# Optimization experiments

Hardware: AMD Instinct MI355X
Metric: run time of the kernel (lower is better)

Reference implementation:

```python
import jax, jax.numpy as jnp
import numpy as np
from jax import lax

WIN = 9  # NCC window per axis (default [9]*3)

# 3x3x3 edge/shape kernels, shape [O=1, I=1, 3, 3, 3]
_LAP = np.zeros((3, 3, 3), np.float32)
_LAP[1, 1, 1] = 6.0
_LAP[0, 1, 1] = _LAP[2, 1, 1] = -1.0
_LAP[1, 0, 1] = _LAP[1, 2, 1] = -1.0
_LAP[1, 1, 0] = _LAP[1, 1, 2] = -1.0
LAP_K = jnp.asarray(_LAP)[None, None]

_row = np.array([[-1.0, 0.0, 1.0], [-2.0, 0.0, 2.0], [-1.0, 0.0, 1.0]], np.float32)
SOBEL_X = jnp.asarray(np.stack([_row, _row, _row], axis=0))[None, None]
_plane = np.array([[-1.0, -2.0, -1.0], [-1.0, -2.0, -1.0], [-1.0, -2.0, -1.0]], np.float32)
SOBEL_Y = jnp.asarray(np.stack([_plane, np.zeros((3, 3), np.float32), -_plane], axis=0))[None, None]
_zp = np.array([[-1.0, -1.0, -1.0], [0.0, 0.0, 0.0], [1.0, 1.0, 1.0]], np.float32)
SOBEL_Z = jnp.asarray(np.stack([_zp, 2.0 * _zp, _zp], axis=0))[None, None]


def conv3d(x, k, pad):
    # x: [N,C,D,H,W], k: [O,I,kd,kh,kw]
    return lax.conv_general_dilated(x, k, (1, 1, 1), [(pad, pad)] * 3)


def box_sum(x, win=WIN):
    # Separable all-ones box filter == dense ones conv (same math, fewer FLOPs)
    pad = win // 2
    for axis in range(3):
        kshape = [1, 1, 1, 1, 1]
        kshape[2 + axis] = win
        k = jnp.ones(kshape, x.dtype)
        padding = [(pad, pad) if a == axis else (0, 0) for a in range(3)]
        x = lax.conv_general_dilated(x, k, (1, 1, 1), padding)
    return x


def ncc_vxm(Ii, Ji, win=WIN):
    win_size = float(win ** 3)
    I2, J2, IJ = Ii * Ii, Ji * Ji, Ii * Ji
    I_sum = box_sum(Ii, win)
    J_sum = box_sum(Ji, win)
    I2_sum = box_sum(I2, win)
    J2_sum = box_sum(J2, win)
    IJ_sum = box_sum(IJ, win)
    u_I = I_sum / win_size
    u_J = J_sum / win_size
    cross = IJ_sum - u_J * I_sum - u_I * J_sum + u_I * u_J * win_size
    I_var = I2_sum - 2.0 * u_I * I_sum + u_I * u_I * win_size
    J_var = J2_sum - 2.0 * u_J * J_sum + u_J * u_J * win_size
    cc = cross * cross / (I_var * J_var + 1e-5)
    return -jnp.mean(cc)


def edge_detection(v):
    return conv3d(v, LAP_K, pad=1)


def shape_detection(v):
    gx = conv3d(v, SOBEL_X, pad=1)
    gy = conv3d(v, SOBEL_Y, pad=1)
    gz = conv3d(v, SOBEL_Z, pad=1)
    return jnp.sqrt(gx * gx + gy * gy + gz * gz)


def setup_inputs() -> dict:
    key = jax.random.key(0)
    k1, k2 = jax.random.split(key)
    shape = (1, 1, 160, 192, 160)
    y_true = jax.random.uniform(k1, shape, dtype=jnp.float32)
    y_pred = jax.random.uniform(k2, shape, dtype=jnp.float32)
    return {"y_true": y_true, "y_pred": y_pred}


def reference(y_true, y_pred):
    loss_orig = ncc_vxm(y_true, y_pred)
    loss_edge = ncc_vxm(edge_detection(y_true), edge_detection(y_pred))
    loss_shape = ncc_vxm(shape_detection(y_true), shape_detection(y_pred))
    return 0.8 * loss_orig + 0.1 * loss_edge + 0.1 * loss_shape
```

## Files before the change

kernel.cpp:

```cpp
#include <hip/hip_runtime.h>
#include <hip/hip_fp16.h>
#include <math.h>

#define DD 160
#define HHH 192
#define WWW 160
constexpr int HW = HHH * WWW;
constexpr int NV = DD * HHH * WWW;
constexpr int W4 = WWW / 4;
constexpr int HC = 4;
constexpr int DC = 4;
constexpr int SC = 5;

constexpr int NB_WH  = (W4 * DD * (HHH / HC)) / 256;
constexpr int NB_SO  = (W4 * HHH * (DD / SC)) / 256;
constexpr int NB_LAP = (NV / 4) / 256;
constexpr int NB_DCC = (W4 * HHH * (DD / DC)) / 256;

__device__ __forceinline__ float4 ldg4(const float* __restrict__ p, int idx, bool ok) {
    float4 z = make_float4(0.f, 0.f, 0.f, 0.f);
    return ok ? *(const float4*)(p + idx) : z;
}

__device__ __forceinline__ void st_h4(__half* __restrict__ t, int idx,
                                      float s0, float s1, float s2, float s3) {
    union { __half2 h2[2]; uint2 u; } pk;
    pk.h2[0] = __floats2half2_rn(s0, s1);
    pk.h2[1] = __floats2half2_rn(s2, s3);
    *(uint2*)(t + idx) = pk.u;
}

__device__ __forceinline__ void ld_h4(const __half* __restrict__ t, int idx, float o[4]) {
    union { __half2 h2[2]; uint2 u; } pk;
    pk.u = *(const uint2*)(t + idx);
    o[0] = __low2float(pk.h2[0]); o[1] = __high2float(pk.h2[0]);
    o[2] = __low2float(pk.h2[1]); o[3] = __high2float(pk.h2[1]);
}

__device__ __forceinline__ void lap_body(int t, const float* __restrict__ a,
                                         const float* __restrict__ b,
                                         __half* __restrict__ oa, __half* __restrict__ ob) {
    int w = (t % W4) * 4;
    int h = (t / W4) % HHH;
    int d = t / (W4 * HHH);
    int idx = (d * HHH + h) * WWW + w;
    bool dok0 = d > 0, dok1 = d < DD - 1, hok0 = h > 0, hok1 = h < HHH - 1;
#pragma unroll
    for (int s = 0; s < 2; s++) {
        const float* p = s ? b : a;
        __half* o = s ? ob : oa;
        float4 c = *(const float4*)(p + idx);
        float m1 = (w > 0) ? p[idx - 1] : 0.f;
        float p4 = (w + 4 < WWW) ? p[idx + 4] : 0.f;
        float4 dm = ldg4(p, idx - HW, dok0);
        float4 dp = ldg4(p, idx + HW, dok1);
        float4 hm = ldg4(p, idx - WWW, hok0);
        float4 hp = ldg4(p, idx + WWW, hok1);
        st_h4(o, idx,
              6.f * c.x - (m1 + c.y + dm.x + dp.x + hm.x + hp.x),
              6.f * c.y - (c.x + c.z + dm.y + dp.y + hm.y + hp.y),
              6.f * c.z - (c.y + c.w + dm.z + dp.z + hm.z + hp.z),
              6.f * c.w - (c.z + p4 + dm.w + dp.w + hm.w + hp.w));
    }
}

__device__ __forceinline__ void sobel_slice(const float* __restrict__ p, int s, int h, int w,
                                            float a1[4], float a2[4], float a3[4]) {
#pragma unroll
    for (int k = 0; k < 4; k++) { a1[k] = 0.f; a2[k] = 0.f; a3[k] = 0.f; }
#pragma unroll
    for (int kh = -1; kh <= 1; kh++) {
        int h2 = h + kh;
        if ((unsigned)h2 < (unsigned)HHH) {
            int rb = (s * HHH + h2) * WWW + w;
            float4 cen = *(const float4*)(p + rb);
            float xm = (w > 0) ? p[rb - 1] : 0.f;
            float xp = (w + 4 < WWW) ? p[rb + 4] : 0.f;
            float xv[6] = {xm, cen.x, cen.y, cen.z, cen.w, xp};
            float smh = (kh == 0) ? 2.f : 1.f;
            float grh = (float)kh;
#pragma unroll
            for (int k = 0; k < 4; k++) {
                float gw = xv[k + 2] - xv[k];
                float pw = xv[k] + xv[k + 1] + xv[k + 2];
                float sw = pw + xv[k + 1];
                a1[k] += smh * gw;
                a2[k] += sw;
                a3[k] += grh * pw;
            }
        }
    }
}

__device__ __forceinline__ void sobel_body(int t, const float* __restrict__ a,
                                           const float* __restrict__ b,
                                           __half* __restrict__ oa, __half* __restrict__ ob) {
    int w = (t % W4) * 4;
    int h = (t / W4) % HHH;
    int c = t / (W4 * HHH);
    int d0 = c * SC;

    float A1[2][3][4], A2[2][3][4], A3[2][3][4];
#pragma unroll
    for (int r = 0; r < 2; r++)
#pragma unroll
        for (int j = 0; j < 3; j++)
#pragma unroll
            for (int k = 0; k < 4; k++) { A1[r][j][k] = 0.f; A2[r][j][k] = 0.f; A3[r][j][k] = 0.f; }

#pragma unroll
    for (int i = 0; i < SC + 2; i++) {
        int s = d0 - 1 + i;
#pragma unroll
        for (int r = 0; r < 2; r++)
#pragma unroll
            for (int k = 0; k < 4; k++) {
                A1[r][0][k] = A1[r][1][k]; A2[r][0][k] = A2[r][1][k]; A3[r][0][k] = A3[r][1][k];
                A1[r][1][k] = A1[r][2][k]; A2[r][1][k] = A2[r][2][k]; A3[r][1][k] = A3[r][2][k];
            }
        if (s >= 0 && s < DD) {
            sobel_slice(a, s, h, w, A1[0][2], A2[0][2], A3[0][2]);
            sobel_slice(b, s, h, w, A1[1][2], A2[1][2], A3[1][2]);
        } else {
#pragma unroll
            for (int r = 0; r < 2; r++)
#pragma unroll
                for (int k = 0; k < 4; k++) { A1[r][2][k] = 0.f; A2[r][2][k] = 0.f; A3[r][2][k] = 0.f; }
        }
        if (i >= 2) {
            int d = s - 1;
            int idx = (d * HHH + h) * WWW + w;
            float va[4], vb[4];
#pragma unroll
            for (int k = 0; k < 4; k++) {
                float gx = A1[0][0][k] + A1[0][1][k] + A1[0][2][k];
                float gy = A2[0][2][k] - A2[0][0][k];
                float gz = A3[0][0][k] + 2.f * A3[0][1][k] + A3[0][2][k];
                va[k] = sqrtf(gx * gx + gy * gy + gz * gz);
                gx = A1[1][0][k] + A1[1][1][k] + A1[1][2][k];
                gy = A2[1][2][k] - A2[1][0][k];
                gz = A3[1][0][k] + 2.f * A3[1][1][k] + A3[1][2][k];
                vb[k] = sqrtf(gx * gx + gy * gy + gz * gz);
            }
            st_h4(oa, idx, va[0], va[1], va[2], va[3]);
            st_h4(ob, idx, vb[0], vb[1], vb[2], vb[3]);
        }
    }
}

__device__ __forceinline__ void q5_from(const float x[12], const float y[12], float q[5][4]) {
    float s0 = 0, s1 = 0, s2 = 0, s3 = 0, s4 = 0;
#pragma unroll
    for (int j = 0; j < 9; j++) {
        s0 += x[j]; s1 += y[j];
        s2 += x[j] * x[j]; s3 += y[j] * y[j]; s4 += x[j] * y[j];
    }
    q[0][0] = s0; q[1][0] = s1; q[2][0] = s2; q[3][0] = s3; q[4][0] = s4;
#pragma unroll
    for (int k = 1; k < 4; k++) {
        q[0][k] = q[0][k - 1] + x[k + 8] - x[k - 1];
        q[1][k] = q[1][k - 1] + y[k + 8] - y[k - 1];
        q[2][k] = q[2][k - 1] + x[k + 8] * x[k + 8] - x[k - 1] * x[k - 1];
        q[3][k] = q[3][k - 1] + y[k + 8] * y[k + 8] - y[k - 1] * y[k - 1];
        q[4][k] = q[4][k - 1] + x[k + 8] * y[k + 8] - x[k - 1] * y[k - 1];
    }
}

__device__ __forceinline__ void ld12(const float* __restrict__ p, int rowbase, int w, float x[12]) {
    bool lo = (w >= 4);
    bool hi = (w + 7 < WWW);
    float4 x0 = ldg4(p, rowbase + w - 4, lo);
    float4 x1 = *(const float4*)(p + rowbase + w);
    float4 x2 = ldg4(p, rowbase + w + 4, hi);
    x[0] = x0.x; x[1] = x0.y; x[2] = x0.z; x[3] = x0.w;
    x[4] = x1.x; x[5] = x1.y; x[6] = x1.z; x[7] = x1.w;
    x[8] = x2.x; x[9] = x2.y; x[10] = x2.z; x[11] = x2.w;
}

__device__ __forceinline__ void ld12(const __half* __restrict__ p, int rowbase, int w, float x[12]) {
    bool lo = (w >= 4);
    bool hi = (w + 7 < WWW);
    union { __half2 h2[2]; uint2 u; } u0, u1, u2;
    uint2 z = make_uint2(0, 0);
    u0.u = lo ? *(const uint2*)(p + rowbase + w - 4) : z;
    u1.u = *(const uint2*)(p + rowbase + w);
    u2.u = hi ? *(const uint2*)(p + rowbase + w + 4) : z;
    x[0] = __low2float(u0.h2[0]); x[1] = __high2float(u0.h2[0]);
    x[2] = __low2float(u0.h2[1]); x[3] = __high2float(u0.h2[1]);
    x[4] = __low2float(u1.h2[0]); x[5] = __high2float(u1.h2[0]);
    x[6] = __low2float(u1.h2[1]); x[7] = __high2float(u1.h2[1]);
    x[8] = __low2float(u2.h2[0]); x[9] = __high2float(u2.h2[0]);
    x[10] = __low2float(u2.h2[1]); x[11] = __high2float(u2.h2[1]);
}

template <typename T>
__device__ __forceinline__ void rowq5(const T* __restrict__ a, const T* __restrict__ b,
                                      int rowbase, int w, float q[5][4]) {
    float x[12], y[12];
    ld12(a, rowbase, w, x);
    ld12(b, rowbase, w, y);
    q5_from(x, y, q);
}

template <typename T>
__device__ void whsum_body(int t, const T* __restrict__ a, const T* __restrict__ b,
                           __half* __restrict__ t0, __half* __restrict__ t1,
                           __half* __restrict__ t2, __half* __restrict__ t3,
                           __half* __restrict__ t4) {
    int w = (t % W4) * 4;
    int d = (t / W4) % DD;
    int c = t / (W4 * DD);
    int h0 = c * HC;

    float S[5][4] = {{0}};
    for (int j = 0; j < 9; j++) {
        int r = h0 - 4 + j;
        if ((unsigned)r < (unsigned)HHH) {
            float q[5][4];
            rowq5(a, b, (d * HHH + r) * WWW, w, q);
#pragma unroll
            for (int qq = 0; qq < 5; qq++)
#pragma unroll
                for (int k = 0; k < 4; k++) S[qq][k] += q[qq][k];
        }
    }
    {
        int idx = (d * HHH + h0) * WWW + w;
        st_h4(t0, idx, S[0][0], S[0][1], S[0][2], S[0][3]);
        st_h4(t1, idx, S[1][0], S[1][1], S[1][2], S[1][3]);
        st_h4(t2, idx, S[2][0], S[2][1], S[2][2], S[2][3]);
        st_h4(t3, idx, S[3][0], S[3][1], S[3][2], S[3][3]);
        st_h4(t4, idx, S[4][0], S[4][1], S[4][2], S[4][3]);
    }
    for (int h = h0 + 1; h < h0 + HC; h++) {
        int rin = h + 4, rout = h - 5;
        if (rin < HHH) {
            float q[5][4];
            rowq5(a, b, (d * HHH + rin) * WWW, w, q);
#pragma unroll
            for (int qq = 0; qq < 5; qq++)
#pragma unroll
                for (int k = 0; k < 4; k++) S[qq][k] += q[qq][k];
        }
        if (rout >= 0) {
            float q[5][4];
            rowq5(a, b, (d * HHH + rout) * WWW, w, q);
#pragma unroll
            for (int qq = 0; qq < 5; qq++)
#pragma unroll
                for (int k = 0; k < 4; k++) S[qq][k] -= q[qq][k];
        }
        int idx = (d * HHH + h) * WWW + w;
        st_h4(t0, idx, S[0][0], S[0][1], S[0][2], S[0][3]);
        st_h4(t1, idx, S[1][0], S[1][1], S[1][2], S[1][3]);
        st_h4(t2, idx, S[2][0], S[2][1], S[2][2], S[2][3]);
        st_h4(t3, idx, S[3][0], S[3][1], S[3][2], S[3][3]);
        st_h4(t4, idx, S[4][0], S[4][1], S[4][2], S[4][3]);
    }
}

__device__ __forceinline__ float cc1(float s0, float s1, float s2, float s3, float s4) {
    const float wsz = 729.0f;
    const float inv = 1.0f / 729.0f;
    float uI = s0 * inv;
    float uJ = s1 * inv;
    float cross = s4 - uJ * s0 - uI * s1 + uI * uJ * wsz;
    float Iv = s2 - 2.0f * uI * s0 + uI * uI * wsz;
    float Jv = s3 - 2.0f * uJ * s1 + uJ * uJ * wsz;
    return cross * cross / (Iv * Jv + 1e-5f);
}

__device__ void dcc_body(int t, const __half* __restrict__ t0, const __half* __restrict__ t1,
                         const __half* __restrict__ t2, const __half* __restrict__ t3,
                         const __half* __restrict__ t4, double* __restrict__ acc, int pair) {
    int w = (t % W4) * 4;
    int h = (t / W4) % HHH;
    int c = t / (W4 * HHH);
    int d0 = c * DC;

    float S[5][4] = {{0}};
    for (int j = 0; j < 9; j++) {
        int r = d0 - 4 + j;
        if ((unsigned)r < (unsigned)DD) {
            int idx = (r * HHH + h) * WWW + w;
            float v[5][4];
            ld_h4(t0, idx, v[0]); ld_h4(t1, idx, v[1]); ld_h4(t2, idx, v[2]);
            ld_h4(t3, idx, v[3]); ld_h4(t4, idx, v[4]);
#pragma unroll
            for (int q = 0; q < 5; q++)
#pragma unroll
                for (int k = 0; k < 4; k++) S[q][k] += v[q][k];
        }
    }
    float local = 0.f;
#pragma unroll
    for (int k = 0; k < 4; k++) local += cc1(S[0][k], S[1][k], S[2][k], S[3][k], S[4][k]);
#pragma unroll
    for (int d = 1; d < DC; d++) {
        int rin = d0 + d + 4, rout = d0 + d - 5;
        if (rin < DD) {
            int idx = (rin * HHH + h) * WWW + w;
            float v[5][4];
            ld_h4(t0, idx, v[0]); ld_h4(t1, idx, v[1]); ld_h4(t2, idx, v[2]);
            ld_h4(t3, idx, v[3]); ld_h4(t4, idx, v[4]);
#pragma unroll
            for (int q = 0; q < 5; q++)
#pragma unroll
                for (int k = 0; k < 4; k++) S[q][k] += v[q][k];
        }
        if (rout >= 0) {
            int idx = (rout * HHH + h) * WWW + w;
            float v[5][4];
            ld_h4(t0, idx, v[0]); ld_h4(t1, idx, v[1]); ld_h4(t2, idx, v[2]);
            ld_h4(t3, idx, v[3]); ld_h4(t4, idx, v[4]);
#pragma unroll
            for (int q = 0; q < 5; q++)
#pragma unroll
                for (int k = 0; k < 4; k++) S[q][k] -= v[q][k];
        }
#pragma unroll
        for (int k = 0; k < 4; k++) local += cc1(S[0][k], S[1][k], S[2][k], S[3][k], S[4][k]);
    }

    for (int off = 32; off > 0; off >>= 1) local += __shfl_down(local, off);
    __shared__ float wsum_[4];
    if ((threadIdx.x & 63) == 0) wsum_[threadIdx.x >> 6] = local;
    __syncthreads();
    if (threadIdx.x == 0) {
        float s = wsum_[0] + wsum_[1] + wsum_[2] + wsum_[3];
        atomicAdd(&acc[pair], (double)s);
    }
}

__global__ void stage1(const float* __restrict__ yt, const float* __restrict__ yp,
                       __half* __restrict__ e1a, __half* __restrict__ e1b,
                       __half* __restrict__ e2a, __half* __restrict__ e2b,
                       __half* __restrict__ ta0, __half* __restrict__ ta1,
                       __half* __restrict__ ta2, __half* __restrict__ ta3,
                       __half* __restrict__ ta4, double* __restrict__ acc) {
    int b = blockIdx.x;
    if (b < NB_WH) {
        whsum_body<float>(b * 256 + threadIdx.x, yt, yp, ta0, ta1, ta2, ta3, ta4);
    } else if (b < NB_WH + NB_SO) {
        sobel_body((b - NB_WH) * 256 + threadIdx.x, yt, yp, e2a, e2b);
    } else if (b < NB_WH + NB_SO + NB_LAP) {
        lap_body((b - NB_WH - NB_SO) * 256 + threadIdx.x, yt, yp, e1a, e1b);
    } else {
        if (threadIdx.x < 3) acc[threadIdx.x] = 0.0;
    }
}

__global__ void stage23(const __half* __restrict__ ea, const __half* __restrict__ eb,
                        __half* __restrict__ o0, __half* __restrict__ o1,
                        __half* __restrict__ o2, __half* __restrict__ o3,
                        __half* __restrict__ o4,
                        const __half* __restrict__ i0, const __half* __restrict__ i1,
                        const __half* __restrict__ i2, const __half* __restrict__ i3,
                        const __half* __restrict__ i4, double* __restrict__ acc, int pair) {
    int b = blockIdx.x;
    if (b < NB_WH) {
        whsum_body<__half>(b * 256 + threadIdx.x, ea, eb, o0, o1, o2, o3, o4);
    } else {
        dcc_body((b - NB_WH) * 256 + threadIdx.x, i0, i1, i2, i3, i4, acc, pair);
    }
}

__global__ void dcc_k(const __half* __restrict__ t0, const __half* __restrict__ t1,
                      const __half* __restrict__ t2, const __half* __restrict__ t3,
                      const __half* __restrict__ t4, double* __restrict__ acc, int pair) {
    dcc_body(blockIdx.x * 256 + threadIdx.x, t0, t1, t2, t3, t4, acc, pair);
}

__global__ void stage2b(const __half* __restrict__ e1a, const __half* __restrict__ e1b,
                        const __half* __restrict__ e2a, const __half* __restrict__ e2b,
                        __half* __restrict__ tB, __half* __restrict__ tC,
                        const __half* __restrict__ tA, double* __restrict__ acc) {
    int b = blockIdx.x;
    size_t nv = (size_t)NV;
    if (b < NB_WH) {
        whsum_body<__half>(b * 256 + threadIdx.x, e1a, e1b,
                           tB, tB + nv, tB + 2 * nv, tB + 3 * nv, tB + 4 * nv);
    } else if (b < 2 * NB_WH) {
        whsum_body<__half>((b - NB_WH) * 256 + threadIdx.x, e2a, e2b,
                           tC, tC + nv, tC + 2 * nv, tC + 3 * nv, tC + 4 * nv);
    } else {
        dcc_body((b - 2 * NB_WH) * 256 + threadIdx.x,
                 tA, tA + nv, tA + 2 * nv, tA + 3 * nv, tA + 4 * nv, acc, 0);
    }
}

__global__ void stage3b(const __half* __restrict__ tB, const __half* __restrict__ tC,
                        double* __restrict__ acc) {
    int b = blockIdx.x;
    size_t nv = (size_t)NV;
    if (b < NB_DCC) {
        dcc_body(b * 256 + threadIdx.x,
                 tB, tB + nv, tB + 2 * nv, tB + 3 * nv, tB + 4 * nv, acc, 1);
    } else {
        dcc_body((b - NB_DCC) * 256 + threadIdx.x,
                 tC, tC + nv, tC + 2 * nv, tC + 3 * nv, tC + 4 * nv, acc, 2);
    }
}

__global__ void finalize_k(const double* __restrict__ acc, float* __restrict__ out) {
    if (threadIdx.x == 0) {
        double v = 0.8 * acc[0] + 0.1 * acc[1] + 0.1 * acc[2];
        out[0] = (float)(-v / (double)NV);
    }
}

extern "C" void kernel_launch(void* const* d_in, const int* in_sizes, int n_in,
                              void* d_out, int out_size, void* d_ws, size_t ws_size,
                              hipStream_t stream) {
    const float* yt = (const float*)d_in[0];
    const float* yp = (const float*)d_in[1];
    float* out = (float*)d_out;

    double* acc = (double*)d_ws;
    __half* base = (__half*)((char*)d_ws + 256);
    size_t nv = (size_t)NV;
    __half* e1a = base + 0 * nv;
    __half* e1b = base + 1 * nv;
    __half* e2a = base + 2 * nv;
    __half* e2b = base + 3 * nv;
    __half* tA = base + 4 * nv;
    __half* tB = base + 9 * nv;
    __half* tC = base + 14 * nv;

    bool wide = ws_size >= 256 + 19 * nv * sizeof(__half);

    dim3 blk(256);

    hipLaunchKernelGGL(stage1, dim3(NB_WH + NB_SO + NB_LAP + 1), blk, 0, stream,
                       yt, yp, e1a, e1b, e2a, e2b,
                       tA, tA + nv, tA + 2 * nv, tA + 3 * nv, tA + 4 * nv, acc);

    if (wide) {
        hipLaunchKernelGGL(stage2b, dim3(2 * NB_WH + NB_DCC), blk, 0, stream,
                           e1a, e1b, e2a, e2b, tB, tC, tA, acc);
        hipLaunchKernelGGL(stage3b, dim3(2 * NB_DCC), blk, 0, stream, tB, tC, acc);
    } else {
        hipLaunchKernelGGL(stage23, dim3(NB_WH + NB_DCC), blk, 0, stream,
                           e1a, e1b,
                           tB, tB + nv, tB + 2 * nv, tB + 3 * nv, tB + 4 * nv,
                           tA, tA + nv, tA + 2 * nv, tA + 3 * nv, tA + 4 * nv,
                           acc, 0);
        hipLaunchKernelGGL(stage23, dim3(NB_WH + NB_DCC), blk, 0, stream,
                           e2a, e2b,
                           tA, tA + nv, tA + 2 * nv, tA + 3 * nv, tA + 4 * nv,
                           tB, tB + nv, tB + 2 * nv, tB + 3 * nv, tB + 4 * nv,
                           acc, 1);
        hipLaunchKernelGGL(dcc_k, dim3(NB_DCC), blk, 0, stream,
                           tA, tA + nv, tA + 2 * nv, tA + 3 * nv, tA + 4 * nv, acc, 2);
    }

    hipLaunchKernelGGL(finalize_k, dim3(1), dim3(1), 0, stream, acc, out);
}
```

Before: 374.3 us.

## Widen per-thread chunks, make sliding-window loads branchless, reorder stage1 blocks

Doubles the D-axis chunk per thread in the correlation pass (DC 4→8) and the Sobel slab (SC 5→8), and has the Laplacian handle 8 voxels per thread with a 16-byte half store. The sliding-window loops over H and D are fully unrolled, and boundary branches become predicated zero loads so the loads can be issued together. Stage1 now schedules the Sobel blocks first. The aim is to cut redundant halo reads and raise memory-level parallelism, at the cost of higher register pressure and fewer blocks, which may lower occupancy.

```diff
diff --git a/kernel.cpp b/kernel.cpp
--- a/kernel.cpp
+++ b/kernel.cpp
@@ -8,13 +8,14 @@
 constexpr int HW = HHH * WWW;
 constexpr int NV = DD * HHH * WWW;
 constexpr int W4 = WWW / 4;
+constexpr int W8 = WWW / 8;
 constexpr int HC = 4;
-constexpr int DC = 4;
-constexpr int SC = 5;
+constexpr int DC = 8;
+constexpr int SC = 8;
 
 constexpr int NB_WH  = (W4 * DD * (HHH / HC)) / 256;
 constexpr int NB_SO  = (W4 * HHH * (DD / SC)) / 256;
-constexpr int NB_LAP = (NV / 4) / 256;
+constexpr int NB_LAP = (NV / 8) / 256;
 constexpr int NB_DCC = (W4 * HHH * (DD / DC)) / 256;
 
 __device__ __forceinline__ float4 ldg4(const float* __restrict__ p, int idx, bool ok) {
@@ -30,9 +31,19 @@
     *(uint2*)(t + idx) = pk.u;
 }
 
-__device__ __forceinline__ void ld_h4(const __half* __restrict__ t, int idx, float o[4]) {
+__device__ __forceinline__ void st_h8(__half* __restrict__ t, int idx, const float s[8]) {
+    union { __half2 h2[4]; uint4 u; } pk;
+    pk.h2[0] = __floats2half2_rn(s[0], s[1]);
+    pk.h2[1] = __floats2half2_rn(s[2], s[3]);
+    pk.h2[2] = __floats2half2_rn(s[4], s[5]);
+    pk.h2[3] = __floats2half2_rn(s[6], s[7]);
+    *(uint4*)(t + idx) = pk.u;
+}
+
+__device__ __forceinline__ void ld_h4g(const __half* __restrict__ t, int idx, bool ok, float o[4]) {
     union { __half2 h2[2]; uint2 u; } pk;
-    pk.u = *(const uint2*)(t + idx);
+    uint2 z = make_uint2(0, 0);
+    pk.u = ok ? *(const uint2*)(t + idx) : z;
     o[0] = __low2float(pk.h2[0]); o[1] = __high2float(pk.h2[0]);
     o[2] = __low2float(pk.h2[1]); o[3] = __high2float(pk.h2[1]);
 }
@@ -40,27 +51,33 @@
 __device__ __forceinline__ void lap_body(int t, const float* __restrict__ a,
                                          const float* __restrict__ b,
                                          __half* __restrict__ oa, __half* __restrict__ ob) {
-    int w = (t % W4) * 4;
-    int h = (t / W4) % HHH;
-    int d = t / (W4 * HHH);
+    int w = (t % W8) * 8;
+    int h = (t / W8) % HHH;
+    int d = t / (W8 * HHH);
     int idx = (d * HHH + h) * WWW + w;
     bool dok0 = d > 0, dok1 = d < DD - 1, hok0 = h > 0, hok1 = h < HHH - 1;
 #pragma unroll
     for (int s = 0; s < 2; s++) {
         const float* p = s ? b : a;
         __half* o = s ? ob : oa;
-        float4 c = *(const float4*)(p + idx);
+        float4 c0 = *(const float4*)(p + idx);
+        float4 c1 = *(const float4*)(p + idx + 4);
         float m1 = (w > 0) ? p[idx - 1] : 0.f;
-        float p4 = (w + 4 < WWW) ? p[idx + 4] : 0.f;
-        float4 dm = ldg4(p, idx - HW, dok0);
-        float4 dp = ldg4(p, idx + HW, dok1);
-        float4 hm = ldg4(p, idx - WWW, hok0);
-        float4 hp = ldg4(p, idx + WWW, hok1);
-        st_h4(o, idx,
-              6.f * c.x - (m1 + c.y + dm.x + dp.x + hm.x + hp.x),
-              6.f * c.y - (c.x + c.z + dm.y + dp.y + hm.y + hp.y),
-              6.f * c.z - (c.y + c.w + dm.z + dp.z + hm.z + hp.z),
-              6.f * c.w - (c.z + p4 + dm.w + dp.w + hm.w + hp.w));
+        float p8 = (w + 8 < WWW) ? p[idx + 8] : 0.f;
+        float4 dm0 = ldg4(p, idx - HW, dok0),      dm1 = ldg4(p, idx + 4 - HW, dok0);
+        float4 dp0 = ldg4(p, idx + HW, dok1),      dp1 = ldg4(p, idx + 4 + HW, dok1);
+        float4 hm0 = ldg4(p, idx - WWW, hok0),     hm1 = ldg4(p, idx + 4 - WWW, hok0);
+        float4 hp0 = ldg4(p, idx + WWW, hok1),     hp1 = ldg4(p, idx + 4 + WWW, hok1);
+        float cv[10] = {m1, c0.x, c0.y, c0.z, c0.w, c1.x, c1.y, c1.z, c1.w, p8};
+        float dmv[8] = {dm0.x, dm0.y, dm0.z, dm0.w, dm1.x, dm1.y, dm1.z, dm1.w};
+        float dpv[8] = {dp0.x, dp0.y, dp0.z, dp0.w, dp1.x, dp1.y, dp1.z, dp1.w};
+        float hmv[8] = {hm0.x, hm0.y, hm0.z, hm0.w, hm1.x, hm1.y, hm1.z, hm1.w};
+        float hpv[8] = {hp0.x, hp0.y, hp0.z, hp0.w, hp1.x, hp1.y, hp1.z, hp1.w};
+        float out[8];
+#pragma unroll
+        for (int k = 0; k < 8; k++)
+            out[k] = 6.f * cv[k + 1] - (cv[k] + cv[k + 2] + dmv[k] + dpv[k] + hmv[k] + hpv[k]);
+        st_h8(o, idx, out);
     }
 }
 
@@ -166,24 +183,26 @@
     }
 }
 
-__device__ __forceinline__ void ld12(const float* __restrict__ p, int rowbase, int w, float x[12]) {
-    bool lo = (w >= 4);
-    bool hi = (w + 7 < WWW);
+__device__ __forceinline__ void ld12(const float* __restrict__ p, int rowbase, int w, bool ok,
+                                     float x[12]) {
+    bool lo = ok && (w >= 4);
+    bool hi = ok && (w + 7 < WWW);
     float4 x0 = ldg4(p, rowbase + w - 4, lo);
-    float4 x1 = *(const float4*)(p + rowbase + w);
+    float4 x1 = ldg4(p, rowbase + w, ok);
     float4 x2 = ldg4(p, rowbase + w + 4, hi);
     x[0] = x0.x; x[1] = x0.y; x[2] = x0.z; x[3] = x0.w;
     x[4] = x1.x; x[5] = x1.y; x[6] = x1.z; x[7] = x1.w;
     x[8] = x2.x; x[9] = x2.y; x[10] = x2.z; x[11] = x2.w;
 }
 
-__device__ __forceinline__ void ld12(const __half* __restrict__ p, int rowbase, int w, float x[12]) {
-    bool lo = (w >= 4);
-    bool hi = (w + 7 < WWW);
+__device__ __forceinline__ void ld12(const __half* __restrict__ p, int rowbase, int w, bool ok,
+                                     float x[12]) {
+    bool lo = ok && (w >= 4);
+    bool hi = ok && (w + 7 < WWW);
     union { __half2 h2[2]; uint2 u; } u0, u1, u2;
     uint2 z = make_uint2(0, 0);
     u0.u = lo ? *(const uint2*)(p + rowbase + w - 4) : z;
-    u1.u = *(const uint2*)(p + rowbase + w);
+    u1.u = ok ? *(const uint2*)(p + rowbase + w) : z;
     u2.u = hi ? *(const uint2*)(p + rowbase + w + 4) : z;
     x[0] = __low2float(u0.h2[0]); x[1] = __high2float(u0.h2[0]);
     x[2] = __low2float(u0.h2[1]); x[3] = __high2float(u0.h2[1]);
@@ -195,10 +214,10 @@
 
 template <typename T>
 __device__ __forceinline__ void rowq5(const T* __restrict__ a, const T* __restrict__ b,
-                                      int rowbase, int w, float q[5][4]) {
+                                      int rowbase, int w, bool ok, float q[5][4]) {
     float x[12], y[12];
-    ld12(a, rowbase, w, x);
-    ld12(b, rowbase, w, y);
+    ld12(a, rowbase, w, ok, x);
+    ld12(b, rowbase, w, ok, y);
     q5_from(x, y, q);
 }
 
@@ -213,16 +232,16 @@
     int h0 = c * HC;
 
     float S[5][4] = {{0}};
+#pragma unroll
     for (int j = 0; j < 9; j++) {
         int r = h0 - 4 + j;
-        if ((unsigned)r < (unsigned)HHH) {
-            float q[5][4];
-            rowq5(a, b, (d * HHH + r) * WWW, w, q);
-#pragma unroll
-            for (int qq = 0; qq < 5; qq++)
-#pragma unroll
-                for (int k = 0; k < 4; k++) S[qq][k] += q[qq][k];
-        }
+        bool ok = (unsigned)r < (unsigned)HHH;
+        float q[5][4];
+        rowq5(a, b, (d * HHH + r) * WWW, w, ok, q);
+#pragma unroll
+        for (int qq = 0; qq < 5; qq++)
+#pragma unroll
+            for (int k = 0; k < 4; k++) S[qq][k] += q[qq][k];
     }
     {
         int idx = (d * HHH + h0) * WWW + w;
@@ -232,24 +251,19 @@
         st_h4(t3, idx, S[3][0], S[3][1], S[3][2], S[3][3]);
         st_h4(t4, idx, S[4][0], S[4][1], S[4][2], S[4][3]);
     }
-    for (int h = h0 + 1; h < h0 + HC; h++) {
+#pragma unroll
+    for (int hh = 1; hh < HC; hh++) {
+        int h = h0 + hh;
         int rin = h + 4, rout = h - 5;
-        if (rin < HHH) {
-            float q[5][4];
-            rowq5(a, b, (d * HHH + rin) * WWW, w, q);
-#pragma unroll
-            for (int qq = 0; qq < 5; qq++)
-#pragma unroll
-                for (int k = 0; k < 4; k++) S[qq][k] += q[qq][k];
-        }
-        if (rout >= 0) {
-            float q[5][4];
-            rowq5(a, b, (d * HHH + rout) * WWW, w, q);
-#pragma unroll
-            for (int qq = 0; qq < 5; qq++)
-#pragma unroll
-                for (int k = 0; k < 4; k++) S[qq][k] -= q[qq][k];
-        }
+        bool oki = rin < HHH;
+        bool oko = rout >= 0;
+        float qi[5][4], qo[5][4];
+        rowq5(a, b, (d * HHH + rin) * WWW, w, oki, qi);
+        rowq5(a, b, (d * HHH + rout) * WWW, w, oko, qo);
+#pragma unroll
+        for (int qq = 0; qq < 5; qq++)
+#pragma unroll
+            for (int k = 0; k < 4; k++) S[qq][k] += qi[qq][k] - qo[qq][k];
         int idx = (d * HHH + h) * WWW + w;
         st_h4(t0, idx, S[0][0], S[0][1], S[0][2], S[0][3]);
         st_h4(t1, idx, S[1][0], S[1][1], S[1][2], S[1][3]);
@@ -279,18 +293,18 @@
     int d0 = c * DC;
 
     float S[5][4] = {{0}};
+#pragma unroll
     for (int j = 0; j < 9; j++) {
         int r = d0 - 4 + j;
-        if ((unsigned)r < (unsigned)DD) {
-            int idx = (r * HHH + h) * WWW + w;
-            float v[5][4];
-            ld_h4(t0, idx, v[0]); ld_h4(t1, idx, v[1]); ld_h4(t2, idx, v[2]);
-            ld_h4(t3, idx, v[3]); ld_h4(t4, idx, v[4]);
-#pragma unroll
-            for (int q = 0; q < 5; q++)
-#pragma unroll
-                for (int k = 0; k < 4; k++) S[q][k] += v[q][k];
-        }
+        bool ok = (unsigned)r < (unsigned)DD;
+        int idx = (r * HHH + h) * WWW + w;
+        float v[5][4];
+        ld_h4g(t0, idx, ok, v[0]); ld_h4g(t1, idx, ok, v[1]); ld_h4g(t2, idx, ok, v[2]);
+        ld_h4g(t3, idx, ok, v[3]); ld_h4g(t4, idx, ok, v[4]);
+#pragma unroll
+        for (int q = 0; q < 5; q++)
+#pragma unroll
+            for (int k = 0; k < 4; k++) S[q][k] += v[q][k];
     }
     float local = 0.f;
 #pragma unroll
@@ -298,26 +312,19 @@
 #pragma unroll
     for (int d = 1; d < DC; d++) {
         int rin = d0 + d + 4, rout = d0 + d - 5;
-        if (rin < DD) {
-            int idx = (rin * HHH + h) * WWW + w;
-            float v[5][4];
-            ld_h4(t0, idx, v[0]); ld_h4(t1, idx, v[1]); ld_h4(t2, idx, v[2]);
-            ld_h4(t3, idx, v[3]); ld_h4(t4, idx, v[4]);
-#pragma unroll
-            for (int q = 0; q < 5; q++)
-#pragma unroll
-                for (int k = 0; k < 4; k++) S[q][k] += v[q][k];
-        }
-        if (rout >= 0) {
-            int idx = (rout * HHH + h) * WWW + w;
-            float v[5][4];
-            ld_h4(t0, idx, v[0]); ld_h4(t1, idx, v[1]); ld_h4(t2, idx, v[2]);
-            ld_h4(t3, idx, v[3]); ld_h4(t4, idx, v[4]);
-#pragma unroll
-            for (int q = 0; q < 5; q++)
-#pragma unroll
-                for (int k = 0; k < 4; k++) S[q][k] -= v[q][k];
-        }
+        bool oki = rin < DD;
+        bool oko = rout >= 0;
+        int idxi = (rin * HHH + h) * WWW + w;
+        int idxo = (rout * HHH + h) * WWW + w;
+        float vi[5][4], vo[5][4];
+        ld_h4g(t0, idxi, oki, vi[0]); ld_h4g(t1, idxi, oki, vi[1]); ld_h4g(t2, idxi, oki, vi[2]);
+        ld_h4g(t3, idxi, oki, vi[3]); ld_h4g(t4, idxi, oki, vi[4]);
+        ld_h4g(t0, idxo, oko, vo[0]); ld_h4g(t1, idxo, oko, vo[1]); ld_h4g(t2, idxo, oko, vo[2]);
+        ld_h4g(t3, idxo, oko, vo[3]); ld_h4g(t4, idxo, oko, vo[4]);
+#pragma unroll
+        for (int q = 0; q < 5; q++)
+#pragma unroll
+            for (int k = 0; k < 4; k++) S[q][k] += vi[q][k] - vo[q][k];
 #pragma unroll
         for (int k = 0; k < 4; k++) local += cc1(S[0][k], S[1][k], S[2][k], S[3][k], S[4][k]);
     }
@@ -339,12 +346,12 @@
                        __half* __restrict__ ta2, __half* __restrict__ ta3,
                        __half* __restrict__ ta4, double* __restrict__ acc) {
     int b = blockIdx.x;
-    if (b < NB_WH) {
-        whsum_body<float>(b * 256 + threadIdx.x, yt, yp, ta0, ta1, ta2, ta3, ta4);
-    } else if (b < NB_WH + NB_SO) {
-        sobel_body((b - NB_WH) * 256 + threadIdx.x, yt, yp, e2a, e2b);
-    } else if (b < NB_WH + NB_SO + NB_LAP) {
-        lap_body((b - NB_WH - NB_SO) * 256 + threadIdx.x, yt, yp, e1a, e1b);
+    if (b < NB_SO) {
+        sobel_body(b * 256 + threadIdx.x, yt, yp, e2a, e2b);
+    } else if (b < NB_SO + NB_WH) {
+        whsum_body<float>((b - NB_SO) * 256 + threadIdx.x, yt, yp, ta0, ta1, ta2, ta3, ta4);
+    } else if (b < NB_SO + NB_WH + NB_LAP) {
+        lap_body((b - NB_SO - NB_WH) * 256 + threadIdx.x, yt, yp, e1a, e1b);
     } else {
         if (threadIdx.x < 3) acc[threadIdx.x] = 0.0;
     }
@@ -431,7 +438,7 @@
 
     dim3 blk(256);
 
-    hipLaunchKernelGGL(stage1, dim3(NB_WH + NB_SO + NB_LAP + 1), blk, 0, stream,
+    hipLaunchKernelGGL(stage1, dim3(NB_SO + NB_WH + NB_LAP + 1), blk, 0, stream,
                        yt, yp, e1a, e1b, e2a, e2b,
                        tA, tA + nv, tA + 2 * nv, tA + 3 * nv, tA + 4 * nv, acc);
 
```

After: 846.5 us. 2.26x slower.
